# Optimization experiments

Hardware: AMD Instinct MI355X
Metric: run time of the kernel (lower is better)

Reference implementation:

```python
import math
import jax, jax.numpy as jnp
import numpy as np

B, N, D, H = 4, 2048, 1024, 16
DK = D // H

def setup_inputs() -> dict:
    key = jax.random.key(0)
    k1, k2, k3 = jax.random.split(key, 3)
    x = jax.random.normal(k1, (B, N, D), dtype=jnp.float32)
    # torch Linear weight is [out,in]; we store transposed [in,out] for x @ W
    w_qkv = jax.random.normal(k2, (D, 3 * D), dtype=jnp.float32) * (1.0 / math.sqrt(D))
    w_out = jax.random.normal(k3, (D, D), dtype=jnp.float32) * (1.0 / math.sqrt(D))
    return {"x": x, "w_qkv": w_qkv, "w_out": w_out}

def reference(x, w_qkv, w_out):
    b, n, d = x.shape
    qkv = x @ w_qkv                                   # [B,N,3D]
    q, k, v = jnp.split(qkv, 3, axis=-1)
    def split_heads(t):
        return t.reshape(b, n, H, DK).transpose(0, 2, 1, 3)  # [B,H,N,DK]
    q, k, v = map(split_heads, (q, k, v))
    scale = 1.0 / math.sqrt(DK)
    attn = jnp.einsum('bhqd,bhkd->bhqk', q, k) * scale  # [B,H,N,N]
    attn = jax.nn.softmax(attn, axis=-1)
    out = jnp.einsum('bhqk,bhkd->bhqd', attn, v)        # [B,H,N,DK]
    out = out.transpose(0, 2, 1, 3).reshape(b, n, d)
    return out @ w_out                                  # dropout p=0 -> identity
```

## Files before the change

### kernel.cpp

```cpp
#include <hip/hip_runtime.h>
#include <hip/hip_bf16.h>

typedef __bf16 bf16;
typedef __bf16 bf16x8 __attribute__((ext_vector_type(8)));
typedef float f32x2 __attribute__((ext_vector_type(2)));
typedef float f32x4 __attribute__((ext_vector_type(4)));
typedef float f32x16 __attribute__((ext_vector_type(16)));
typedef short s16x4 __attribute__((ext_vector_type(4)));

#define GLDS16(gp, lp) __builtin_amdgcn_global_load_lds( \
    (const __attribute__((address_space(1))) void*)(gp), \
    (__attribute__((address_space(3))) void*)(lp), 16, 0, 0)

__device__ __forceinline__ bf16 f2bf(float f) {
    unsigned u = __builtin_bit_cast(unsigned, f);
    u = (u + 0x7FFFu + ((u >> 16) & 1u)) >> 16;
    unsigned short s = (unsigned short)u;
    return __builtin_bit_cast(bf16, s);
}
__device__ __forceinline__ void store_c(float* p, float v) { *p = v; }
__device__ __forceinline__ void store_c(bf16*  p, float v) { *p = f2bf(v); }

__device__ __forceinline__ float exp2_fast(float x) {
    float r; asm("v_exp_f32 %0, %1" : "=v"(r) : "v"(x)); return r;
}
__device__ __forceinline__ unsigned cvt_pk_bf16(float lo, float hi) {
    unsigned r;
    asm("v_cvt_pk_bf16_f32 %0, %1, %2" : "=v"(r) : "v"(lo), "v"(hi));
    return r;
}
__device__ __forceinline__ void permlane32_swap(unsigned &a, unsigned &b) {
    asm("v_permlane32_swap_b32 %0, %1" : "+v"(a), "+v"(b));
}
__device__ __forceinline__ s16x4 ds_tr16(unsigned addr) {
    s16x4 d;
    asm volatile("ds_read_b64_tr_b16 %0, %1" : "=v"(d) : "v"(addr));
    return d;
}

__global__ __launch_bounds__(256) void cvt_f32_bf16(
    const float* __restrict__ in, bf16* __restrict__ out, int n8)
{
    int i = blockIdx.x * 256 + threadIdx.x;
    if (i >= n8) return;
    f32x4 a = *(const f32x4*)(in + (size_t)i * 8);
    f32x4 b = *(const f32x4*)(in + (size_t)i * 8 + 4);
    bf16x8 o;
    #pragma unroll
    for (int j = 0; j < 4; ++j) { o[j] = f2bf(a[j]); o[4 + j] = f2bf(b[j]); }
    *(bf16x8*)(out + (size_t)i * 8) = o;
}

template <typename TC>
__global__ __launch_bounds__(256) void gemm_glds(
    const bf16* __restrict__ A, const bf16* __restrict__ B, TC* __restrict__ C,
    int M, int N, int K)
{
    __shared__ alignas(16) bf16 As[128 * 32];
    __shared__ alignas(16) bf16 Bs[32 * 128];

    const int tid  = threadIdx.x;
    const int wv   = tid >> 6;
    const int lane = tid & 63;
    const int lr   = lane & 15;
    const int kb   = lane >> 4;
    const int wr   = wv >> 1, wc = wv & 1;
    const int brow = blockIdx.y * 128;
    const int bcol = blockIdx.x * 128;

    f32x4 acc[4][4] = {};

    const int ar0 = wv * 16 + (lane >> 2);
    const int ac0 = (lane & 3) * 8;

    const int bL   = wv * 1024 + lane * 16;
    const int bs0  = bL >> 7;
    const int b_r  = (bL & 127) >> 5;
    const int b_c0 = (bL & 31) >> 1;

    for (int k0 = 0; k0 < K; k0 += 32) {
        __syncthreads();
        #pragma unroll
        for (int t = 0; t < 2; ++t)
            GLDS16(A + (size_t)(brow + t * 64 + ar0) * K + k0 + ac0,
                   &As[t * 2048 + wv * 512]);
        #pragma unroll
        for (int t = 0; t < 2; ++t) {
            int s = bs0 + t * 32;
            GLDS16(B + (size_t)(k0 + (s >> 3) * 4 + b_r) * N + bcol + (s & 7) * 16 + b_c0,
                   &Bs[t * 2048 + wv * 512]);
        }
        __syncthreads();

        bf16x8 af[4], bfr[4];
        #pragma unroll
        for (int m = 0; m < 4; ++m)
            af[m] = *(const bf16x8*)&As[(wr * 64 + m * 16 + lr) * 32 + kb * 8];
        {
            s16x4 tr[8];
            const unsigned bsb = (unsigned)(uintptr_t)Bs + kb * 2048 + lr * 8;
            #pragma unroll
            for (int nt = 0; nt < 4; ++nt) {
                unsigned a = bsb + (wc * 4 + nt) * 128;
                tr[nt * 2]     = ds_tr16(a);
                tr[nt * 2 + 1] = ds_tr16(a + 1024);
            }
            asm volatile("s_waitcnt lgkmcnt(0)" ::: "memory");
            __builtin_amdgcn_sched_barrier(0);
            #pragma unroll
            for (int nt = 0; nt < 4; ++nt) {
                union { bf16x8 f; s16x4 h[2]; } u;
                u.h[0] = tr[nt * 2]; u.h[1] = tr[nt * 2 + 1];
                bfr[nt] = u.f;
            }
        }
        #pragma unroll
        for (int m = 0; m < 4; ++m)
            #pragma unroll
            for (int n = 0; n < 4; ++n)
                acc[m][n] = __builtin_amdgcn_mfma_f32_16x16x32_bf16(af[m], bfr[n], acc[m][n], 0, 0, 0);
    }

    #pragma unroll
    for (int m = 0; m < 4; ++m)
        #pragma unroll
        for (int n = 0; n < 4; ++n)
            #pragma unroll
            for (int r = 0; r < 4; ++r) {
                int row = brow + wr * 64 + m * 16 + kb * 4 + r;
                int col = bcol + wc * 64 + n * 16 + lr;
                store_c(&C[(size_t)row * N + col], acc[m][n][r]);
            }
}

__global__ __launch_bounds__(256) void attn_mfma32(
    const bf16* __restrict__ qkv, bf16* __restrict__ attn_out)
{
    constexpr int NSEQ = 2048, DM = 1024, LD = 3072, KVB = 64, QB = 128;
    constexpr int NT = NSEQ / KVB;
    constexpr float THR = 11.5f;
    __shared__ alignas(16) bf16 KsBuf[2][64][72];
    __shared__ alignas(16) bf16 VsBuf[2][4096];

    const int tid = threadIdx.x;
    const int wv = tid >> 6, lane = tid & 63;
    const int l31 = lane & 31;
    const int hi_ = lane >> 5;
    const int g16 = (lane >> 4) & 1;
    const int l16 = lane & 15;

    const int wg  = blockIdx.x;
    const int xcd = wg & 7, j = wg >> 3;
    const int bh  = xcd * 8 + (j & 7);
    const int q0  = (j >> 3) * QB;
    const int b = bh >> 4, h = bh & 15;

    const bf16* qbase = qkv + (size_t)(b * NSEQ) * LD + h * 64;
    const bf16* kbase = qbase + DM;
    const bf16* vbase = qbase + 2 * DM;

    bf16x8 qf[4];
    {
        const float QSC = 0.125f * 1.44269504f;
        const bf16* qp = qbase + (size_t)(q0 + wv * 32 + l31) * LD + hi_ * 8;
        #pragma unroll
        for (int ds = 0; ds < 4; ++ds) {
            bf16x8 t = *(const bf16x8*)(qp + ds * 16);
            #pragma unroll
            for (int e = 0; e < 8; ++e) t[e] = f2bf((float)t[e] * QSC);
            qf[ds] = t;
        }
    }

    f32x16 o0 = {}, o1 = {};
    float mrow = -INFINITY, lsum = 0.f;

    const int krow = tid >> 2, kcol = (tid & 3) * 16;

    auto vload = [&](int j0, int L) {
        int kq = L >> 8, cb = (L >> 6) & 3, rr = (L >> 4) & 3, c0 = L & 15;
        return *(const bf16x8*)(vbase + (size_t)(j0 + kq * 4 + rr) * LD + cb * 16 + c0);
    };

    bf16x8 kr0 = *(const bf16x8*)(kbase + (size_t)krow * LD + kcol);
    bf16x8 kr1 = *(const bf16x8*)(kbase + (size_t)krow * LD + kcol + 8);
    bf16x8 vr0 = vload(0, tid * 8);
    bf16x8 vr1 = vload(0, 2048 + tid * 8);

    for (int kt = 0; kt < NT; ++kt) {
        const int cur = kt & 1;
        bf16 (*Ks)[72] = KsBuf[cur];
        bf16 *Vs       = VsBuf[cur];
        const unsigned vb = (unsigned)(uintptr_t)Vs;

        *(bf16x8*)&Ks[krow][kcol]       = kr0;
        *(bf16x8*)&Ks[krow][kcol + 8]   = kr1;
        *(bf16x8*)(Vs + tid * 8)        = vr0;
        *(bf16x8*)(Vs + 2048 + tid * 8) = vr1;
        __syncthreads();

        {
            const int jn = (kt + 1 < NT ? kt + 1 : kt) * KVB;
            kr0 = *(const bf16x8*)(kbase + (size_t)(jn + krow) * LD + kcol);
            kr1 = *(const bf16x8*)(kbase + (size_t)(jn + krow) * LD + kcol + 8);
            vr0 = vload(jn, tid * 8);
            vr1 = vload(jn, 2048 + tid * 8);
        }

        f32x16 sT0 = {}, sT1 = {};
        __builtin_amdgcn_s_setprio(1);
        #pragma unroll
        for (int ds = 0; ds < 4; ++ds) {
            bf16x8 kf = *(const bf16x8*)&Ks[l31][ds * 16 + hi_ * 8];
            sT0 = __builtin_amdgcn_mfma_f32_32x32x16_bf16(kf, qf[ds], sT0, 0, 0, 0);
        }
        #pragma unroll
        for (int ds = 0; ds < 4; ++ds) {
            bf16x8 kf = *(const bf16x8*)&Ks[32 + l31][ds * 16 + hi_ * 8];
            sT1 = __builtin_amdgcn_mfma_f32_32x32x16_bf16(kf, qf[ds], sT1, 0, 0, 0);
        }
        __builtin_amdgcn_s_setprio(0);

        float pm = fmaxf(sT0[0], sT0[1]);
        #pragma unroll
        for (int r = 2; r < 16; r += 2) pm = fmaxf(fmaxf(pm, sT0[r]), sT0[r + 1]);
        #pragma unroll
        for (int r = 0; r < 16; r += 2) pm = fmaxf(fmaxf(pm, sT1[r]), sT1[r + 1]);
        pm = fmaxf(pm, __shfl_xor(pm, 32));
        if (!__all(pm <= mrow + THR)) {
            const float mn = fmaxf(mrow, pm);
            const float corr = exp2_fast(mrow - mn);
            mrow = mn;
            lsum *= corr;
            #pragma unroll
            for (int r = 0; r < 16; ++r) { o0[r] *= corr; o1[r] *= corr; }
        }
        #pragma unroll
        for (int r = 0; r < 16; ++r) sT0[r] = exp2_fast(sT0[r] - mrow);
        #pragma unroll
        for (int r = 0; r < 16; ++r) sT1[r] = exp2_fast(sT1[r] - mrow);
        f32x2 ps2 = {0.f, 0.f};
        #pragma unroll
        for (int r = 0; r < 16; r += 2) {
            ps2 += (f32x2){sT0[r], sT0[r + 1]};
            ps2 += (f32x2){sT1[r], sT1[r + 1]};
        }
        float ps = ps2[0] + ps2[1];
        ps += __shfl_xor(ps, 32);
        lsum += ps;

        unsigned w0[8], w1[8];
        #pragma unroll
        for (int j2 = 0; j2 < 8; ++j2) {
            w0[j2] = cvt_pk_bf16(sT0[2 * j2], sT0[2 * j2 + 1]);
            w1[j2] = cvt_pk_bf16(sT1[2 * j2], sT1[2 * j2 + 1]);
        }
        bf16x8 pf[4];
        #pragma unroll
        for (int ks = 0; ks < 4; ++ks) {
            const int jb = 4 * (ks & 1);
            unsigned a0 = (ks >> 1) ? w1[jb]     : w0[jb];
            unsigned b0 = (ks >> 1) ? w1[jb + 2] : w0[jb + 2];
            unsigned a1 = (ks >> 1) ? w1[jb + 1] : w0[jb + 1];
            unsigned b1 = (ks >> 1) ? w1[jb + 3] : w0[jb + 3];
            permlane32_swap(a0, b0);
            permlane32_swap(a1, b1);
            union { bf16x8 f; unsigned w[4]; } u;
            u.w[0] = a0; u.w[1] = a1; u.w[2] = b0; u.w[3] = b1;
            pf[ks] = u.f;
        }

        #pragma unroll
        for (int dt = 0; dt < 2; ++dt) {
            s16x4 t[8];
            #pragma unroll
            for (int ks = 0; ks < 4; ++ks) {
                unsigned a = vb + ks * 2048 + hi_ * 1024 + dt * 256 + g16 * 128 + l16 * 8;
                t[ks * 2]     = ds_tr16(a);
                t[ks * 2 + 1] = ds_tr16(a + 512);
            }
            asm volatile("s_waitcnt lgkmcnt(0)" ::: "memory");
            __builtin_amdgcn_sched_barrier(0);
            __builtin_amdgcn_s_setprio(1);
            #pragma unroll
            for (int ks = 0; ks < 4; ++ks) {
                union { bf16x8 f; s16x4 h[2]; } u;
                u.h[0] = t[ks * 2]; u.h[1] = t[ks * 2 + 1];
                if (dt == 0) o0 = __builtin_amdgcn_mfma_f32_32x32x16_bf16(u.f, pf[ks], o0, 0, 0, 0);
                else         o1 = __builtin_amdgcn_mfma_f32_32x32x16_bf16(u.f, pf[ks], o1, 0, 0, 0);
            }
            __builtin_amdgcn_s_setprio(0);
        }
    }

    bf16 (*Os)[72] = (bf16 (*)[72])&KsBuf[0][0][0];
    const float inv = 1.f / lsum;
    __syncthreads();
    #pragma unroll
    for (int r = 0; r < 16; ++r) {
        const int d0 = (r & 3) + 8 * (r >> 2) + 4 * hi_;
        Os[wv * 32 + l31][d0]      = f2bf(o0[r] * inv);
        Os[wv * 32 + l31][32 + d0] = f2bf(o1[r] * inv);
    }
    __syncthreads();
    {
        const int row = tid >> 1, c0 = (tid & 1) * 32;
        bf16* op = attn_out + (size_t)(b * NSEQ + q0 + row) * DM + h * 64 + c0;
        #pragma unroll
        for (int e = 0; e < 4; ++e)
            *(bf16x8*)(op + e * 8) = *(const bf16x8*)&Os[row][c0 + e * 8];
    }
}

extern "C" void kernel_launch(void* const* d_in, const int* in_sizes, int n_in,
                              void* d_out, int out_size, void* d_ws, size_t ws_size,
                              hipStream_t stream) {
    const float* x     = (const float*)d_in[0];
    const float* w_qkv = (const float*)d_in[1];
    const float* w_out = (const float*)d_in[2];
    float* out = (float*)d_out;

    bf16* x_bf    = (bf16*)d_out;
    bf16* qkv     = (bf16*)d_ws;
    bf16* wqkv_bf = qkv + (size_t)8192 * 3072;
    bf16* attnb   = wqkv_bf;
    bf16* wo_bf   = (bf16*)d_ws;

    cvt_f32_bf16<<<4096, 256, 0, stream>>>(x, x_bf, 8192 * 1024 / 8);
    cvt_f32_bf16<<<1536, 256, 0, stream>>>(w_qkv, wqkv_bf, 1024 * 3072 / 8);
    gemm_glds<bf16><<<dim3(3072 / 128, 8192 / 128), 256, 0, stream>>>(
        x_bf, wqkv_bf, qkv, 8192, 3072, 1024);
    attn_mfma32<<<1024, 256, 0, stream>>>(qkv, attnb);
    cvt_f32_bf16<<<512, 256, 0, stream>>>(w_out, wo_bf, 1024 * 1024 / 8);
    gemm_glds<float><<<dim3(1024 / 128, 8192 / 128), 256, 0, stream>>>(
        attnb, wo_bf, out, 8192, 1024, 1024);
}
```

Measured before the change: 223.8 us.

## Triple-buffer GEMM LDS tiles with async global-to-LDS prefetch two stages ahead

Measured after the change: 218.6 us. 2.3% less time.

```diff
diff --git a/kernel.cpp b/kernel.cpp
--- a/kernel.cpp
+++ b/kernel.cpp
@@ -52,12 +52,12 @@
 }
 
 template <typename TC>
-__global__ __launch_bounds__(256) void gemm_glds(
+__global__ __launch_bounds__(256) void gemm_pipe(
     const bf16* __restrict__ A, const bf16* __restrict__ B, TC* __restrict__ C,
     int M, int N, int K)
 {
-    __shared__ alignas(16) bf16 As[128 * 32];
-    __shared__ alignas(16) bf16 Bs[32 * 128];
+    __shared__ alignas(16) bf16 As[3][128 * 32];
+    __shared__ alignas(16) bf16 Bs[3][32 * 128];
 
     const int tid  = threadIdx.x;
     const int wv   = tid >> 6;
@@ -78,27 +78,40 @@
     const int b_r  = (bL & 127) >> 5;
     const int b_c0 = (bL & 31) >> 1;
 
-    for (int k0 = 0; k0 < K; k0 += 32) {
-        __syncthreads();
+    auto stage = [&](int buf, int k0) {
         #pragma unroll
         for (int t = 0; t < 2; ++t)
             GLDS16(A + (size_t)(brow + t * 64 + ar0) * K + k0 + ac0,
-                   &As[t * 2048 + wv * 512]);
+                   &As[buf][t * 2048 + wv * 512]);
         #pragma unroll
         for (int t = 0; t < 2; ++t) {
             int s = bs0 + t * 32;
             GLDS16(B + (size_t)(k0 + (s >> 3) * 4 + b_r) * N + bcol + (s & 7) * 16 + b_c0,
-                   &Bs[t * 2048 + wv * 512]);
-        }
-        __syncthreads();
-
+                   &Bs[buf][t * 2048 + wv * 512]);
+        }
+    };
+
+    stage(0, 0);
+    stage(1, 32);
+
+    const int KT = K >> 5;
+    for (int kt = 0; kt < KT; ++kt) {
+        if (kt + 1 < KT) asm volatile("s_waitcnt vmcnt(4)" ::: "memory");
+        else             asm volatile("s_waitcnt vmcnt(0)" ::: "memory");
+        __builtin_amdgcn_s_barrier();
+        __builtin_amdgcn_sched_barrier(0);
+
+        if (kt + 2 < KT) stage((kt + 2) % 3, (kt + 2) << 5);
+
+        const int cur = kt % 3;
+        const bf16* Ab = As[cur];
         bf16x8 af[4], bfr[4];
         #pragma unroll
         for (int m = 0; m < 4; ++m)
-            af[m] = *(const bf16x8*)&As[(wr * 64 + m * 16 + lr) * 32 + kb * 8];
+            af[m] = *(const bf16x8*)&Ab[(wr * 64 + m * 16 + lr) * 32 + kb * 8];
         {
             s16x4 tr[8];
-            const unsigned bsb = (unsigned)(uintptr_t)Bs + kb * 2048 + lr * 8;
+            const unsigned bsb = (unsigned)(uintptr_t)Bs[cur] + kb * 2048 + lr * 8;
             #pragma unroll
             for (int nt = 0; nt < 4; ++nt) {
                 unsigned a = bsb + (wc * 4 + nt) * 128;
@@ -114,11 +127,13 @@
                 bfr[nt] = u.f;
             }
         }
+        __builtin_amdgcn_s_setprio(1);
         #pragma unroll
         for (int m = 0; m < 4; ++m)
             #pragma unroll
             for (int n = 0; n < 4; ++n)
                 acc[m][n] = __builtin_amdgcn_mfma_f32_16x16x32_bf16(af[m], bfr[n], acc[m][n], 0, 0, 0);
+        __builtin_amdgcn_s_setprio(0);
     }
 
     #pragma unroll
@@ -328,10 +343,10 @@
 
     cvt_f32_bf16<<<4096, 256, 0, stream>>>(x, x_bf, 8192 * 1024 / 8);
     cvt_f32_bf16<<<1536, 256, 0, stream>>>(w_qkv, wqkv_bf, 1024 * 3072 / 8);
-    gemm_glds<bf16><<<dim3(3072 / 128, 8192 / 128), 256, 0, stream>>>(
+    gemm_pipe<bf16><<<dim3(3072 / 128, 8192 / 128), 256, 0, stream>>>(
         x_bf, wqkv_bf, qkv, 8192, 3072, 1024);
     attn_mfma32<<<1024, 256, 0, stream>>>(qkv, attnb);
     cvt_f32_bf16<<<512, 256, 0, stream>>>(w_out, wo_bf, 1024 * 1024 / 8);
-    gemm_glds<float><<<dim3(1024 / 128, 8192 / 128), 256, 0, stream>>>(
+    gemm_pipe<float><<<dim3(1024 / 128, 8192 / 128), 256, 0, stream>>>(
         attnb, wo_bf, out, 8192, 1024, 1024);
 }
```
